# Optimization experiments

Measured on AMD Instinct MI355X. Metric: run time of the kernel, lower is better.

The kernel has to match this reference:

```python
import jax, jax.numpy as jnp
import numpy as np

D = 1024
H = 16
DH = D // H  # 64
B, S = 4, 1024


def setup_inputs() -> dict:
    key = jax.random.key(0)
    ks = jax.random.split(key, 7)
    sequences = jax.random.normal(ks[0], (B, S, D), dtype=jnp.float32)
    scale = 1.0 / np.sqrt(DH)
    Wq = jax.random.normal(ks[1], (H, DH, DH), dtype=jnp.float32) * scale
    Wk = jax.random.normal(ks[2], (H, DH, DH), dtype=jnp.float32) * scale
    Wv = jax.random.normal(ks[3], (H, DH, DH), dtype=jnp.float32) * scale
    bq = jax.random.normal(ks[4], (H, DH), dtype=jnp.float32) * 0.01
    bk = jax.random.normal(ks[5], (H, DH), dtype=jnp.float32) * 0.01
    bv = jax.random.normal(ks[6], (H, DH), dtype=jnp.float32) * 0.01
    return {"sequences": sequences, "Wq": Wq, "Wk": Wk, "Wv": Wv,
            "bq": bq, "bk": bk, "bv": bv}


def reference(sequences, Wq, Wk, Wv, bq, bk, bv):
    b, s, d = sequences.shape
    x = sequences.reshape(b, s, H, DH)  # split channels into heads
    # per-head Linear: y = x @ W.T + b (torch convention)
    q = jnp.einsum('bshd,hed->bshe', x, Wq) + bq
    k = jnp.einsum('bshd,hed->bshe', x, Wk) + bk
    v = jnp.einsum('bshd,hed->bshe', x, Wv) + bv
    inv_sqrt_dh = jnp.asarray(1.0 / np.sqrt(DH), dtype=sequences.dtype)
    scores = jnp.einsum('bshe,bthe->bhst', q, k) * inv_sqrt_dh  # [B,H,S,S]
    attn = jax.nn.softmax(scores, axis=-1)
    out = jnp.einsum('bhst,bthe->bshe', attn, v)  # [B,S,H,DH]
    return out.reshape(b, s, d)  # hstack of heads == reshape here
```

## Files before the change

kernel.cpp:

```cpp
#include <hip/hip_runtime.h>

#define H 16
#define DH 64
#define BB 4
#define SS 1024
#define DD 1024
#define LDP 72

typedef __attribute__((ext_vector_type(8))) short bf16x8;
typedef __attribute__((ext_vector_type(4))) float f32x4;
typedef __attribute__((ext_vector_type(4))) unsigned int u32x4;
typedef _Float16 f16x4 __attribute__((ext_vector_type(4)));
typedef __fp16 hf16x2 __attribute__((ext_vector_type(2)));

#define QSCALE 0.18033688011112042f

__device__ __forceinline__ unsigned short f2bf(float f) {
    union { float f; unsigned u; } v; v.f = f;
    unsigned u = v.u;
    return (unsigned short)((u + 0x7FFFu + ((u >> 16) & 1u)) >> 16);
}

__device__ __forceinline__ unsigned short f2h(float f) {
    union { _Float16 h; unsigned short u; } v;
    v.h = (_Float16)f;
    return v.u;
}

__device__ __forceinline__ void pack8(unsigned short* dst, f32x4 a, f32x4 b) {
    unsigned u0 = (unsigned)f2bf(a[0]) | ((unsigned)f2bf(a[1]) << 16);
    unsigned u1 = (unsigned)f2bf(a[2]) | ((unsigned)f2bf(a[3]) << 16);
    unsigned u2 = (unsigned)f2bf(b[0]) | ((unsigned)f2bf(b[1]) << 16);
    unsigned u3 = (unsigned)f2bf(b[2]) | ((unsigned)f2bf(b[3]) << 16);
    u32x4 v = {u0, u1, u2, u3};
    *(u32x4*)dst = v;
}

__global__ __launch_bounds__(256) void wprep_kernel(
    const float* __restrict__ Wq, const float* __restrict__ Wk,
    const float* __restrict__ Wv, unsigned short* __restrict__ Wp)
{
    const int idx = (blockIdx.x * 256 + threadIdx.x) * 16;
    const int NW = H * DH * DH;
    const float* src;
    float scale = 1.0f;
    int off = idx;
    if (idx < NW) { src = Wq; scale = QSCALE; }
    else if (idx < 2 * NW) { src = Wk; off = idx - NW; }
    else { src = Wv; off = idx - 2 * NW; }
    f32x4 f0 = *(const f32x4*)(src + off);
    f32x4 f1 = *(const f32x4*)(src + off + 4);
    f32x4 f2 = *(const f32x4*)(src + off + 8);
    f32x4 f3 = *(const f32x4*)(src + off + 12);
    f0 *= scale; f1 *= scale; f2 *= scale; f3 *= scale;
    pack8(Wp + idx, f0, f1);
    pack8(Wp + idx + 8, f2, f3);
}

__global__ __launch_bounds__(256) void qkv_kernel(
    const float* __restrict__ x, const unsigned short* __restrict__ Wp,
    const float* __restrict__ bq, const float* __restrict__ bk,
    const float* __restrict__ bv,
    unsigned short* __restrict__ Qg, unsigned short* __restrict__ Kg,
    unsigned short* __restrict__ VTg)
{
    __shared__ __align__(16) unsigned short Xb[64 * LDP];
    __shared__ __align__(16) unsigned short Wb0[64 * LDP];
    __shared__ __align__(16) unsigned short Wb1[64 * LDP];
    __shared__ __align__(16) unsigned short Wb2[64 * LDP];

    const int bid = blockIdx.x;
    const int sc = bid & 15, h = (bid >> 4) & 15, b = bid >> 8;
    const int s0 = sc * 64;
    const int tid = threadIdx.x;

    {
        const int s = tid >> 2, dg = (tid & 3) * 16;
        const float* src = x + ((size_t)(b * SS + s0 + s)) * DD + h * DH + dg;
        f32x4 f0 = *(const f32x4*)(src);
        f32x4 f1 = *(const f32x4*)(src + 4);
        f32x4 f2 = *(const f32x4*)(src + 8);
        f32x4 f3 = *(const f32x4*)(src + 12);
        pack8(&Xb[s * LDP + dg], f0, f1);
        pack8(&Xb[s * LDP + dg + 8], f2, f3);
    }
    {
        const int e = tid >> 2, dg = (tid & 3) * 16;
        const int NW = H * DH * DH;
        const unsigned short* wsrc = Wp + h * DH * DH + e * DH + dg;
        *(u32x4*)&Wb0[e * LDP + dg] = *(const u32x4*)(wsrc);
        *(u32x4*)&Wb0[e * LDP + dg + 8] = *(const u32x4*)(wsrc + 8);
        *(u32x4*)&Wb1[e * LDP + dg] = *(const u32x4*)(wsrc + NW);
        *(u32x4*)&Wb1[e * LDP + dg + 8] = *(const u32x4*)(wsrc + NW + 8);
        *(u32x4*)&Wb2[e * LDP + dg] = *(const u32x4*)(wsrc + 2 * NW);
        *(u32x4*)&Wb2[e * LDP + dg + 8] = *(const u32x4*)(wsrc + 2 * NW + 8);
    }
    __syncthreads();

    const int lane = tid & 63, w = tid >> 6;
    const int l15 = lane & 15, quad = lane >> 4;

    f32x4 acc[3][4];
#pragma unroll
    for (int m = 0; m < 3; m++)
#pragma unroll
        for (int nt = 0; nt < 4; nt++) acc[m][nt] = (f32x4){0.f, 0.f, 0.f, 0.f};

#pragma unroll
    for (int k2 = 0; k2 < 2; k2++) {
        bf16x8 a = *(const bf16x8*)&Xb[(w * 16 + l15) * LDP + k2 * 32 + quad * 8];
#pragma unroll
        for (int nt = 0; nt < 4; nt++) {
            const int boff = (nt * 16 + l15) * LDP + k2 * 32 + quad * 8;
            bf16x8 b0 = *(const bf16x8*)&Wb0[boff];
            acc[0][nt] = __builtin_amdgcn_mfma_f32_16x16x32_bf16(a, b0, acc[0][nt], 0, 0, 0);
            bf16x8 b1 = *(const bf16x8*)&Wb1[boff];
            acc[1][nt] = __builtin_amdgcn_mfma_f32_16x16x32_bf16(a, b1, acc[1][nt], 0, 0, 0);
            bf16x8 b2 = *(const bf16x8*)&Wb2[boff];
            acc[2][nt] = __builtin_amdgcn_mfma_f32_16x16x32_bf16(a, b2, acc[2][nt], 0, 0, 0);
        }
    }
    __syncthreads();

#pragma unroll
    for (int nt = 0; nt < 4; nt++) {
        const int e = nt * 16 + l15;
        const float bqs = bq[h * DH + e] * QSCALE;
        const float bks = bk[h * DH + e];
        const float bvs = bv[h * DH + e];
#pragma unroll
        for (int r = 0; r < 4; r++) {
            const int srow = w * 16 + quad * 4 + r;
            Xb[srow * LDP + e]  = f2bf(acc[0][nt][r] + bqs);
            Wb0[srow * LDP + e] = f2bf(acc[1][nt][r] + bks);
            Wb1[e * LDP + srow] = f2h(acc[2][nt][r] + bvs);
        }
    }
    __syncthreads();
    {
        const size_t bh = (size_t)(b * H + h);
        const int row = tid >> 2, cg = (tid & 3) * 16;
        unsigned short* qdst = Qg + (bh * SS + s0 + row) * DH + cg;
        *(u32x4*)qdst = *(const u32x4*)&Xb[row * LDP + cg];
        *(u32x4*)(qdst + 8) = *(const u32x4*)&Xb[row * LDP + cg + 8];
        unsigned short* kdst = Kg + (bh * SS + s0 + row) * DH + cg;
        *(u32x4*)kdst = *(const u32x4*)&Wb0[row * LDP + cg];
        *(u32x4*)(kdst + 8) = *(const u32x4*)&Wb0[row * LDP + cg + 8];
        unsigned short* vdst = VTg + (bh * DH + row) * SS + s0 + cg;
        *(u32x4*)vdst = *(const u32x4*)&Wb1[row * LDP + cg];
        *(u32x4*)(vdst + 8) = *(const u32x4*)&Wb1[row * LDP + cg + 8];
    }
}

__global__ __launch_bounds__(256) void attn_kernel(
    const unsigned short* __restrict__ Qg, const unsigned short* __restrict__ Kg,
    const unsigned short* __restrict__ VTg, float* __restrict__ out)
{
    __shared__ __align__(16) unsigned short Klds[64 * LDP];
    __shared__ __align__(16) unsigned short VTlds[64 * LDP];

    const int bid = blockIdx.x;
    const int qt = bid & 15, h = (bid >> 4) & 15, b = bid >> 8;
    const int tid = threadIdx.x;
    const int lane = tid & 63, w = tid >> 6;
    const int l15 = lane & 15, quad = lane >> 4;
    const size_t bh = (size_t)(b * H + h);

    bf16x8 aQ[2];
    {
        const unsigned short* qp =
            Qg + (bh * SS + qt * 64 + w * 16 + l15) * DH + quad * 8;
        aQ[0] = *(const bf16x8*)(qp);
        aQ[1] = *(const bf16x8*)(qp + 32);
    }

    f32x4 accO[4];
#pragma unroll
    for (int et = 0; et < 4; et++) accO[et] = (f32x4){0.f, 0.f, 0.f, 0.f};
    float m_st = -1e30f, l_st = 0.f;

    for (int kt = 0; kt < 16; kt++) {
        __syncthreads();
#pragma unroll
        for (int it = 0; it < 2; it++) {
            const int item = it * 256 + tid;
            const int row = item >> 3, c8 = (item & 7) * 8;
            u32x4 kv = *(const u32x4*)(Kg + (bh * SS + kt * 64 + row) * DH + c8);
            *(u32x4*)&Klds[row * LDP + c8] = kv;
            u32x4 vv = *(const u32x4*)(VTg + (bh * DH + row) * SS + kt * 64 + c8);
            *(u32x4*)&VTlds[row * LDP + c8] = vv;
        }
        __syncthreads();

        f32x4 sc[4];
#pragma unroll
        for (int nt = 0; nt < 4; nt++) {
            f32x4 z = {0.f, 0.f, 0.f, 0.f};
#pragma unroll
            for (int k2 = 0; k2 < 2; k2++) {
                bf16x8 aK = *(const bf16x8*)&Klds[(nt * 16 + l15) * LDP + k2 * 32 + quad * 8];
                z = __builtin_amdgcn_mfma_f32_16x16x32_bf16(aK, aQ[k2], z, 0, 0, 0);
            }
            sc[nt] = z;
        }

        float lm = -1e30f;
#pragma unroll
        for (int nt = 0; nt < 4; nt++)
#pragma unroll
            for (int r = 0; r < 4; r++) lm = fmaxf(lm, sc[nt][r]);
        lm = fmaxf(lm, __shfl_xor(lm, 16));
        lm = fmaxf(lm, __shfl_xor(lm, 32));
        const float mn = fmaxf(m_st, lm);
        const float alpha = exp2f(m_st - mn);
        m_st = mn;

        float p[4][4];
        float rs = 0.f;
#pragma unroll
        for (int nt = 0; nt < 4; nt++)
#pragma unroll
            for (int r = 0; r < 4; r++) {
                p[nt][r] = exp2f(sc[nt][r] - mn);
                rs += p[nt][r];
            }
        rs += __shfl_xor(rs, 16);
        rs += __shfl_xor(rs, 32);
        l_st = l_st * alpha + rs;

        f16x4 pf[4];
#pragma unroll
        for (int nt = 0; nt < 4; nt++) {
            hf16x2 lo = __builtin_amdgcn_cvt_pkrtz(p[nt][0], p[nt][1]);
            hf16x2 hi = __builtin_amdgcn_cvt_pkrtz(p[nt][2], p[nt][3]);
            pf[nt][0] = (_Float16)lo[0]; pf[nt][1] = (_Float16)lo[1];
            pf[nt][2] = (_Float16)hi[0]; pf[nt][3] = (_Float16)hi[1];
        }

#pragma unroll
        for (int et = 0; et < 4; et++) accO[et] *= alpha;

#pragma unroll
        for (int et = 0; et < 4; et++) {
#pragma unroll
            for (int nt = 0; nt < 4; nt++) {
                f16x4 aV = *(const f16x4*)&VTlds[(et * 16 + l15) * LDP + nt * 16 + quad * 4];
                accO[et] = __builtin_amdgcn_mfma_f32_16x16x16f16(aV, pf[nt], accO[et], 0, 0, 0);
            }
        }
    }

    const float inv = 1.0f / l_st;
    const int srow = qt * 64 + w * 16 + l15;
    float* op = out + ((size_t)b * SS + srow) * DD + h * DH;
#pragma unroll
    for (int et = 0; et < 4; et++) {
        f32x4 v = accO[et] * inv;
        *(f32x4*)(op + et * 16 + quad * 4) = v;
    }
}

extern "C" void kernel_launch(void* const* d_in, const int* in_sizes, int n_in,
                              void* d_out, int out_size, void* d_ws, size_t ws_size,
                              hipStream_t stream) {
    const float* x  = (const float*)d_in[0];
    const float* Wq = (const float*)d_in[1];
    const float* Wk = (const float*)d_in[2];
    const float* Wv = (const float*)d_in[3];
    const float* bq = (const float*)d_in[4];
    const float* bk = (const float*)d_in[5];
    const float* bv = (const float*)d_in[6];

    const size_t NE = (size_t)BB * H * SS * DH;
    unsigned short* Qg  = (unsigned short*)d_ws;
    unsigned short* Kg  = Qg + NE;
    unsigned short* VTg = Kg + NE;
    unsigned short* Wp  = VTg + NE;

    wprep_kernel<<<48, 256, 0, stream>>>(Wq, Wk, Wv, Wp);
    qkv_kernel<<<BB * H * (SS / 64), 256, 0, stream>>>(x, Wp, bq, bk, bv,
                                                       Qg, Kg, VTg);
    attn_kernel<<<BB * H * (SS / 64), 256, 0, stream>>>(Qg, Kg, VTg, (float*)d_out);
}
```

Baseline: 133.3 us.

## Double-buffer K/V tiles with async global-to-LDS loads and XOR-swizzled layouts

Stores K, V^T and the packed weights in global memory as contiguous 64x64 tiles with an XOR swizzle, so tiles can be copied straight into LDS with global_load_lds. Drops the padded LDS stride in favour of the swizzle to avoid bank conflicts. The attention loop now double-buffers K/V tiles, prefetching the next tile while the current one is computed, which removes one barrier per iteration. Attention blocks are reordered so consecutive blocks hit different (batch, head) pairs. In exchange the global layouts become tile-specific and correctness depends on the barrier also waiting for the async copies.

```diff
diff --git a/kernel.cpp b/kernel.cpp
--- a/kernel.cpp
+++ b/kernel.cpp
@@ -5,7 +5,6 @@
 #define BB 4
 #define SS 1024
 #define DD 1024
-#define LDP 72
 
 typedef __attribute__((ext_vector_type(8))) short bf16x8;
 typedef __attribute__((ext_vector_type(4))) float f32x4;
@@ -36,25 +35,36 @@
     *(u32x4*)dst = v;
 }
 
+__device__ __forceinline__ void async_cp1k(const unsigned short* g,
+                                           unsigned short* l, int lane) {
+    __builtin_amdgcn_global_load_lds(
+        (const __attribute__((address_space(1))) unsigned int*)(g + lane * 8),
+        (__attribute__((address_space(3))) unsigned int*)l, 16, 0, 0);
+}
+
 __global__ __launch_bounds__(256) void wprep_kernel(
     const float* __restrict__ Wq, const float* __restrict__ Wk,
     const float* __restrict__ Wv, unsigned short* __restrict__ Wp)
 {
-    const int idx = (blockIdx.x * 256 + threadIdx.x) * 16;
-    const int NW = H * DH * DH;
-    const float* src;
-    float scale = 1.0f;
-    int off = idx;
-    if (idx < NW) { src = Wq; scale = QSCALE; }
-    else if (idx < 2 * NW) { src = Wk; off = idx - NW; }
-    else { src = Wv; off = idx - 2 * NW; }
-    f32x4 f0 = *(const f32x4*)(src + off);
-    f32x4 f1 = *(const f32x4*)(src + off + 4);
-    f32x4 f2 = *(const f32x4*)(src + off + 8);
-    f32x4 f3 = *(const f32x4*)(src + off + 12);
+    const int tg = blockIdx.x * 256 + threadIdx.x;
+    const int r = tg >> 2, part = tg & 3;
+    const int e = r & 63, hm = r >> 6;
+    const int m = hm % 3, h = hm / 3;
+    const float* src = (m == 0 ? Wq : (m == 1 ? Wk : Wv)) +
+                       (size_t)(h * 64 + e) * 64 + part * 16;
+    const float scale = (m == 0) ? QSCALE : 1.0f;
+    f32x4 f0 = ((const f32x4*)src)[0];
+    f32x4 f1 = ((const f32x4*)src)[1];
+    f32x4 f2 = ((const f32x4*)src)[2];
+    f32x4 f3 = ((const f32x4*)src)[3];
     f0 *= scale; f1 *= scale; f2 *= scale; f3 *= scale;
-    pack8(Wp + idx, f0, f1);
-    pack8(Wp + idx + 8, f2, f3);
+    unsigned short tmp[16];
+    pack8(tmp, f0, f1);
+    pack8(tmp + 8, f2, f3);
+    unsigned short* dst = Wp + (size_t)(hm * 64 + e) * 64;
+    const int c0 = part * 2, sw = e & 7;
+    *(u32x4*)(dst + (c0 ^ sw) * 8)       = *(const u32x4*)tmp;
+    *(u32x4*)(dst + ((c0 + 1) ^ sw) * 8) = *(const u32x4*)(tmp + 8);
 }
 
 __global__ __launch_bounds__(256) void qkv_kernel(
@@ -64,41 +74,40 @@
     unsigned short* __restrict__ Qg, unsigned short* __restrict__ Kg,
     unsigned short* __restrict__ VTg)
 {
-    __shared__ __align__(16) unsigned short Xb[64 * LDP];
-    __shared__ __align__(16) unsigned short Wb0[64 * LDP];
-    __shared__ __align__(16) unsigned short Wb1[64 * LDP];
-    __shared__ __align__(16) unsigned short Wb2[64 * LDP];
+    __shared__ __align__(16) unsigned short Xl[4096];
+    __shared__ __align__(16) unsigned short Wl[12288];
 
     const int bid = blockIdx.x;
     const int sc = bid & 15, h = (bid >> 4) & 15, b = bid >> 8;
     const int s0 = sc * 64;
     const int tid = threadIdx.x;
-
-    {
-        const int s = tid >> 2, dg = (tid & 3) * 16;
-        const float* src = x + ((size_t)(b * SS + s0 + s)) * DD + h * DH + dg;
-        f32x4 f0 = *(const f32x4*)(src);
-        f32x4 f1 = *(const f32x4*)(src + 4);
-        f32x4 f2 = *(const f32x4*)(src + 8);
-        f32x4 f3 = *(const f32x4*)(src + 12);
-        pack8(&Xb[s * LDP + dg], f0, f1);
-        pack8(&Xb[s * LDP + dg + 8], f2, f3);
-    }
-    {
-        const int e = tid >> 2, dg = (tid & 3) * 16;
-        const int NW = H * DH * DH;
-        const unsigned short* wsrc = Wp + h * DH * DH + e * DH + dg;
-        *(u32x4*)&Wb0[e * LDP + dg] = *(const u32x4*)(wsrc);
-        *(u32x4*)&Wb0[e * LDP + dg + 8] = *(const u32x4*)(wsrc + 8);
-        *(u32x4*)&Wb1[e * LDP + dg] = *(const u32x4*)(wsrc + NW);
-        *(u32x4*)&Wb1[e * LDP + dg + 8] = *(const u32x4*)(wsrc + NW + 8);
-        *(u32x4*)&Wb2[e * LDP + dg] = *(const u32x4*)(wsrc + 2 * NW);
-        *(u32x4*)&Wb2[e * LDP + dg + 8] = *(const u32x4*)(wsrc + 2 * NW + 8);
+    const int lane = tid & 63, w = tid >> 6;
+
+    {
+        const unsigned short* wbase = Wp + (size_t)h * 12288;
+#pragma unroll
+        for (int sub = 0; sub < 6; sub++) {
+            const int off = w * 3072 + sub * 512;
+            async_cp1k(wbase + off, &Wl[off], lane);
+        }
+    }
+    {
+        const int s = tid >> 2, part = tid & 3;
+        const float* src = x + ((size_t)(b * SS + s0 + s)) * DD + h * DH + part * 16;
+        f32x4 f0 = ((const f32x4*)src)[0];
+        f32x4 f1 = ((const f32x4*)src)[1];
+        f32x4 f2 = ((const f32x4*)src)[2];
+        f32x4 f3 = ((const f32x4*)src)[3];
+        unsigned short tmp[16];
+        pack8(tmp, f0, f1);
+        pack8(tmp + 8, f2, f3);
+        const int c0 = part * 2, sws = s & 7;
+        *(u32x4*)&Xl[s * 64 + (c0 ^ sws) * 8]       = *(const u32x4*)tmp;
+        *(u32x4*)&Xl[s * 64 + ((c0 + 1) ^ sws) * 8] = *(const u32x4*)(tmp + 8);
     }
     __syncthreads();
 
-    const int lane = tid & 63, w = tid >> 6;
-    const int l15 = lane & 15, quad = lane >> 4;
+    const int l15 = lane & 15, quad = lane >> 4, sw = l15 & 7;
 
     f32x4 acc[3][4];
 #pragma unroll
@@ -108,15 +117,16 @@
 
 #pragma unroll
     for (int k2 = 0; k2 < 2; k2++) {
-        bf16x8 a = *(const bf16x8*)&Xb[(w * 16 + l15) * LDP + k2 * 32 + quad * 8];
+        const int csw = (((k2 << 2) | quad) ^ sw) * 8;
+        bf16x8 a = *(const bf16x8*)&Xl[(w * 16 + l15) * 64 + csw];
 #pragma unroll
         for (int nt = 0; nt < 4; nt++) {
-            const int boff = (nt * 16 + l15) * LDP + k2 * 32 + quad * 8;
-            bf16x8 b0 = *(const bf16x8*)&Wb0[boff];
+            const int boff = (nt * 16 + l15) * 64 + csw;
+            bf16x8 b0 = *(const bf16x8*)&Wl[boff];
             acc[0][nt] = __builtin_amdgcn_mfma_f32_16x16x32_bf16(a, b0, acc[0][nt], 0, 0, 0);
-            bf16x8 b1 = *(const bf16x8*)&Wb1[boff];
+            bf16x8 b1 = *(const bf16x8*)&Wl[4096 + boff];
             acc[1][nt] = __builtin_amdgcn_mfma_f32_16x16x32_bf16(a, b1, acc[1][nt], 0, 0, 0);
-            bf16x8 b2 = *(const bf16x8*)&Wb2[boff];
+            bf16x8 b2 = *(const bf16x8*)&Wl[8192 + boff];
             acc[2][nt] = __builtin_amdgcn_mfma_f32_16x16x32_bf16(a, b2, acc[2][nt], 0, 0, 0);
         }
     }
@@ -131,24 +141,25 @@
 #pragma unroll
         for (int r = 0; r < 4; r++) {
             const int srow = w * 16 + quad * 4 + r;
-            Xb[srow * LDP + e]  = f2bf(acc[0][nt][r] + bqs);
-            Wb0[srow * LDP + e] = f2bf(acc[1][nt][r] + bks);
-            Wb1[e * LDP + srow] = f2h(acc[2][nt][r] + bvs);
+            Xl[srow * 64 + e]        = f2bf(acc[0][nt][r] + bqs);
+            Wl[srow * 64 + e]        = f2bf(acc[1][nt][r] + bks);
+            Wl[4096 + e * 64 + srow] = f2h(acc[2][nt][r] + bvs);
         }
     }
     __syncthreads();
     {
         const size_t bh = (size_t)(b * H + h);
-        const int row = tid >> 2, cg = (tid & 3) * 16;
+        const int row = tid >> 2, part = tid & 3;
+        const int cg = part * 16, c0 = part * 2, swr = row & 7;
         unsigned short* qdst = Qg + (bh * SS + s0 + row) * DH + cg;
-        *(u32x4*)qdst = *(const u32x4*)&Xb[row * LDP + cg];
-        *(u32x4*)(qdst + 8) = *(const u32x4*)&Xb[row * LDP + cg + 8];
-        unsigned short* kdst = Kg + (bh * SS + s0 + row) * DH + cg;
-        *(u32x4*)kdst = *(const u32x4*)&Wb0[row * LDP + cg];
-        *(u32x4*)(kdst + 8) = *(const u32x4*)&Wb0[row * LDP + cg + 8];
-        unsigned short* vdst = VTg + (bh * DH + row) * SS + s0 + cg;
-        *(u32x4*)vdst = *(const u32x4*)&Wb1[row * LDP + cg];
-        *(u32x4*)(vdst + 8) = *(const u32x4*)&Wb1[row * LDP + cg + 8];
+        *(u32x4*)qdst       = *(const u32x4*)&Xl[row * 64 + cg];
+        *(u32x4*)(qdst + 8) = *(const u32x4*)&Xl[row * 64 + cg + 8];
+        unsigned short* kbase = Kg + (bh * 16 + sc) * 4096 + row * 64;
+        *(u32x4*)(kbase + (c0 ^ swr) * 8)       = *(const u32x4*)&Wl[row * 64 + c0 * 8];
+        *(u32x4*)(kbase + ((c0 + 1) ^ swr) * 8) = *(const u32x4*)&Wl[row * 64 + c0 * 8 + 8];
+        unsigned short* vbase = VTg + (bh * 16 + sc) * 4096 + row * 64;
+        *(u32x4*)(vbase + (c0 ^ swr) * 8)       = *(const u32x4*)&Wl[4096 + row * 64 + c0 * 8];
+        *(u32x4*)(vbase + ((c0 + 1) ^ swr) * 8) = *(const u32x4*)&Wl[4096 + row * 64 + c0 * 8 + 8];
     }
 }
 
@@ -156,24 +167,35 @@
     const unsigned short* __restrict__ Qg, const unsigned short* __restrict__ Kg,
     const unsigned short* __restrict__ VTg, float* __restrict__ out)
 {
-    __shared__ __align__(16) unsigned short Klds[64 * LDP];
-    __shared__ __align__(16) unsigned short VTlds[64 * LDP];
+    __shared__ __align__(16) unsigned short Kl[2][4096];
+    __shared__ __align__(16) unsigned short Vl[2][4096];
 
     const int bid = blockIdx.x;
-    const int qt = bid & 15, h = (bid >> 4) & 15, b = bid >> 8;
+    const int bh = bid & 63, qt = bid >> 6;
+    const int h = bh & 15, b = bh >> 4;
     const int tid = threadIdx.x;
     const int lane = tid & 63, w = tid >> 6;
-    const int l15 = lane & 15, quad = lane >> 4;
-    const size_t bh = (size_t)(b * H + h);
+    const int l15 = lane & 15, quad = lane >> 4, sw = l15 & 7;
+
+    const unsigned short* Kt = Kg + (size_t)bh * 16 * 4096;
+    const unsigned short* Vt = VTg + (size_t)bh * 16 * 4096;
 
     bf16x8 aQ[2];
     {
         const unsigned short* qp =
-            Qg + (bh * SS + qt * 64 + w * 16 + l15) * DH + quad * 8;
+            Qg + ((size_t)bh * SS + qt * 64 + w * 16 + l15) * DH + quad * 8;
         aQ[0] = *(const bf16x8*)(qp);
         aQ[1] = *(const bf16x8*)(qp + 32);
     }
 
+    {
+        const int off = w * 1024;
+        async_cp1k(Kt + off,       &Kl[0][off],       lane);
+        async_cp1k(Kt + off + 512, &Kl[0][off + 512], lane);
+        async_cp1k(Vt + off,       &Vl[0][off],       lane);
+        async_cp1k(Vt + off + 512, &Vl[0][off + 512], lane);
+    }
+
     f32x4 accO[4];
 #pragma unroll
     for (int et = 0; et < 4; et++) accO[et] = (f32x4){0.f, 0.f, 0.f, 0.f};
@@ -181,16 +203,19 @@
 
     for (int kt = 0; kt < 16; kt++) {
         __syncthreads();
-#pragma unroll
-        for (int it = 0; it < 2; it++) {
-            const int item = it * 256 + tid;
-            const int row = item >> 3, c8 = (item & 7) * 8;
-            u32x4 kv = *(const u32x4*)(Kg + (bh * SS + kt * 64 + row) * DH + c8);
-            *(u32x4*)&Klds[row * LDP + c8] = kv;
-            u32x4 vv = *(const u32x4*)(VTg + (bh * DH + row) * SS + kt * 64 + c8);
-            *(u32x4*)&VTlds[row * LDP + c8] = vv;
-        }
-        __syncthreads();
+        const unsigned short* Kc = Kl[kt & 1];
+        const unsigned short* Vc = Vl[kt & 1];
+        if (kt < 15) {
+            unsigned short* Kn = Kl[(kt + 1) & 1];
+            unsigned short* Vn = Vl[(kt + 1) & 1];
+            const unsigned short* kg = Kt + (kt + 1) * 4096;
+            const unsigned short* vg = Vt + (kt + 1) * 4096;
+            const int off = w * 1024;
+            async_cp1k(kg + off,       Kn + off,       lane);
+            async_cp1k(kg + off + 512, Kn + off + 512, lane);
+            async_cp1k(vg + off,       Vn + off,       lane);
+            async_cp1k(vg + off + 512, Vn + off + 512, lane);
+        }
 
         f32x4 sc[4];
 #pragma unroll
@@ -198,7 +223,8 @@
             f32x4 z = {0.f, 0.f, 0.f, 0.f};
 #pragma unroll
             for (int k2 = 0; k2 < 2; k2++) {
-                bf16x8 aK = *(const bf16x8*)&Klds[(nt * 16 + l15) * LDP + k2 * 32 + quad * 8];
+                bf16x8 aK = *(const bf16x8*)
+                    &Kc[(nt * 16 + l15) * 64 + ((((k2 << 2) | quad)) ^ sw) * 8];
                 z = __builtin_amdgcn_mfma_f32_16x16x32_bf16(aK, aQ[k2], z, 0, 0, 0);
             }
             sc[nt] = z;
@@ -244,7 +270,9 @@
         for (int et = 0; et < 4; et++) {
 #pragma unroll
             for (int nt = 0; nt < 4; nt++) {
-                f16x4 aV = *(const f16x4*)&VTlds[(et * 16 + l15) * LDP + nt * 16 + quad * 4];
+                const int c = 2 * nt + (quad >> 1);
+                f16x4 aV = *(const f16x4*)
+                    &Vc[(et * 16 + l15) * 64 + (c ^ sw) * 8 + (quad & 1) * 4];
                 accO[et] = __builtin_amdgcn_mfma_f32_16x16x16f16(aV, pf[nt], accO[et], 0, 0, 0);
             }
         }
```

Result: no change. 132.6 us (-0.5%).
